# Performance work log

Measured on AMD Instinct MI355X. Metric: run time of the kernel, lower is better.

## Reference

```python
import jax, jax.numpy as jnp
import numpy as np

L, H, C, DH, FF = 6, 8, 512, 64, 2048
B, T, S = 64, 128, 128
EPS = 1e-5


def setup_inputs() -> dict:
    key = jax.random.key(0)
    ks = jax.random.split(key, 20)
    sc = 0.02
    def w(k, shape):
        return jax.random.normal(k, shape, dtype=jnp.float32) * sc
    inp = {
        "x": jax.random.normal(ks[0], (B, T, C), dtype=jnp.float32),
        "encoder_output": jax.random.normal(ks[1], (B, S, C), dtype=jnp.float32),
        # per-head self-attention projections, stacked over layers and heads
        "sa_wq": w(ks[2], (L, H, C, DH)), "sa_bq": w(ks[3], (L, H, DH)),
        "sa_wk": w(ks[4], (L, H, C, DH)), "sa_bk": w(ks[5], (L, H, DH)),
        "sa_wv": w(ks[6], (L, H, C, DH)), "sa_bv": w(ks[7], (L, H, DH)),
        # per-head cross-attention projections
        "ca_wq": w(ks[8], (L, H, C, DH)), "ca_bq": w(ks[9], (L, H, DH)),
        "ca_wk": w(ks[10], (L, H, C, DH)), "ca_bk": w(ks[11], (L, H, DH)),
        "ca_wv": w(ks[12], (L, H, C, DH)), "ca_bv": w(ks[13], (L, H, DH)),
        # feed-forward
        "ff_w1": w(ks[14], (L, C, FF)), "ff_b1": w(ks[15], (L, FF)),
        "ff_w2": w(ks[16], (L, FF, C)), "ff_b2": w(ks[17], (L, C)),
    }
    return inp


def _layer_norm_2d(x):
    # F.layer_norm(x, (T, C)): normalize jointly over last two dims, no affine
    mu = jnp.mean(x, axis=(1, 2), keepdims=True)
    var = jnp.var(x, axis=(1, 2), keepdims=True)
    return (x - mu) * jax.lax.rsqrt(var + EPS)


def _mha(qx, kvx, wq, bq, wk, bk, wv, bv):
    # wq/wk/wv: [H, C, DH]; per-head projections, vectorized over heads.
    q = jnp.einsum("btc,hcd->bhtd", qx, wq) + bq[:, None, :]
    k = jnp.einsum("bsc,hcd->bhsd", kvx, wk) + bk[:, None, :]
    v = jnp.einsum("bsc,hcd->bhsd", kvx, wv) + bv[:, None, :]
    scores = jax.nn.softmax(jnp.einsum("bhtd,bhsd->bhts", q, k) * (DH ** -0.5), axis=-1)
    out = jnp.einsum("bhts,bhsd->bhtd", scores, v)
    b, h, t, d = out.shape  # concat heads along feature dim
    return out.transpose(0, 2, 1, 3).reshape(b, t, h * d)


def reference(x, encoder_output, sa_wq, sa_bq, sa_wk, sa_bk, sa_wv, sa_bv,
              ca_wq, ca_bq, ca_wk, ca_bk, ca_wv, ca_bv,
              ff_w1, ff_b1, ff_w2, ff_b2):
    for l in range(L):
        # masked MHA (note: original code never applies the causal mask)
        x = x + _mha(x, x, sa_wq[l], sa_bq[l], sa_wk[l], sa_bk[l], sa_wv[l], sa_bv[l])
        x = _layer_norm_2d(x)
        # cross attention: q from decoder, k/v from encoder output
        x = x + _mha(x, encoder_output, ca_wq[l], ca_bq[l], ca_wk[l], ca_bk[l], ca_wv[l], ca_bv[l])
        x = _layer_norm_2d(x)
        # feed-forward
        h = jax.nn.relu(jnp.einsum("btc,cf->btf", x, ff_w1[l]) + ff_b1[l])
        x = x + (jnp.einsum("btf,fc->btc", h, ff_w2[l]) + ff_b2[l])
        x = _layer_norm_2d(x)
    return x
```

## Files before the change

kernel.cpp:

```cpp
#include <hip/hip_runtime.h>
#include <hip/hip_bf16.h>


typedef __bf16 bf16;
typedef bf16 bf16x8 __attribute__((ext_vector_type(8)));
typedef float f32x4 __attribute__((ext_vector_type(4)));

#define MFMA16(a, b, c) __builtin_amdgcn_mfma_f32_16x16x32_bf16(a, b, c, 0, 0, 0)

#define GLL16(gsrc, ldst)                                                          \
    __builtin_amdgcn_global_load_lds(                                              \
        (const __attribute__((address_space(1))) void*)(gsrc),                     \
        (__attribute__((address_space(3))) void*)(ldst), 16, 0, 0)

static constexpr int L_ = 6, C_ = 512, FF_ = 2048;
static constexpr int B_ = 64, T_ = 128;
static constexpr int M_ = B_ * T_;
static constexpr float LNINV = 1.f / 65536.f;
static constexpr float EPS_ = 1e-5f;

__global__ __launch_bounds__(256) void zero_part(float* __restrict__ p) {
    for (int i = threadIdx.x; i < 18 * 64 * 2; i += 256) p[i] = 0.f;
}

__global__ __launch_bounds__(256) void init_x(
    const float* __restrict__ xin, float* __restrict__ y, bf16* __restrict__ yb)
{
    const size_t i = ((size_t)blockIdx.x * 256 + threadIdx.x) * 8;
    float4 f0 = *(const float4*)(xin + i);
    float4 f1 = *(const float4*)(xin + i + 4);
    *(float4*)(y + i) = f0;
    *(float4*)(y + i + 4) = f1;
    bf16x8 v = {(bf16)f0.x, (bf16)f0.y, (bf16)f0.z, (bf16)f0.w,
                (bf16)f1.x, (bf16)f1.y, (bf16)f1.z, (bf16)f1.w};
    *(bf16x8*)(yb + i) = v;
}

__global__ __launch_bounds__(256) void to_bf16(
    const float* __restrict__ in, bf16* __restrict__ out)
{
    const size_t i = ((size_t)blockIdx.x * 256 + threadIdx.x) * 8;
    float4 f0 = *(const float4*)(in + i);
    float4 f1 = *(const float4*)(in + i + 4);
    bf16x8 v = {(bf16)f0.x, (bf16)f0.y, (bf16)f0.z, (bf16)f0.w,
                (bf16)f1.x, (bf16)f1.y, (bf16)f1.z, (bf16)f1.w};
    *(bf16x8*)(out + i) = v;
}

__global__ __launch_bounds__(256) void transpose_f32_bf16(
    const float* __restrict__ src, bf16* __restrict__ dst, int R, int C)
{
    __shared__ alignas(16) float t[64][68];
    const int r0 = blockIdx.y * 64, c0 = blockIdx.x * 64;
    const int tr = threadIdx.x >> 4;
    const int tc = (threadIdx.x & 15) * 4;
#pragma unroll
    for (int ro = 0; ro < 64; ro += 16)
        *(float4*)&t[tr + ro][tc] = *(const float4*)(src + (size_t)(r0 + tr + ro) * C + c0 + tc);
    __syncthreads();
    const int wc = (threadIdx.x & 7) * 8;
#pragma unroll
    for (int po = 0; po < 2; ++po) {
        const int oc = (threadIdx.x >> 3) + po * 32;
        bf16x8 v;
#pragma unroll
        for (int j = 0; j < 8; ++j) v[j] = (bf16)t[wc + j][oc];
        *(bf16x8*)(dst + (size_t)(c0 + oc) * R + r0 + wc) = v;
    }
}

__global__ __launch_bounds__(256) void head_repack(
    const float* __restrict__ sa_wq, const float* __restrict__ sa_wk,
    const float* __restrict__ sa_wv, const float* __restrict__ ca_wq,
    const float* __restrict__ ca_wk, const float* __restrict__ ca_wv,
    bf16* __restrict__ Wsa, bf16* __restrict__ Wcaq, bf16* __restrict__ Wcakv)
{
    __shared__ alignas(16) float t[64][68];
    const int z = blockIdx.z;
    const int type = z / 48, rem = z % 48, l = rem >> 3, h = rem & 7;
    const float* srcs[6] = {sa_wq, sa_wk, sa_wv, ca_wq, ca_wk, ca_wv};
    const float* s = srcs[type] + (size_t)(l * 8 + h) * 512 * 64;
    bf16* d;
    if (type < 3)       d = Wsa   + ((size_t)l * 1536 + type * 512 + h * 64) * 512;
    else if (type == 3) d = Wcaq  + ((size_t)l * 512 + h * 64) * 512;
    else                d = Wcakv + ((size_t)l * 1024 + (type - 4) * 512 + h * 64) * 512;
    const int r0 = blockIdx.y * 64;
    const int tr = threadIdx.x >> 4;
    const int tc = (threadIdx.x & 15) * 4;
#pragma unroll
    for (int ro = 0; ro < 64; ro += 16)
        *(float4*)&t[tr + ro][tc] = *(const float4*)(s + (size_t)(r0 + tr + ro) * 64 + tc);
    __syncthreads();
    const int wc = (threadIdx.x & 7) * 8;
#pragma unroll
    for (int po = 0; po < 2; ++po) {
        const int oc = (threadIdx.x >> 3) + po * 32;
        bf16x8 v;
#pragma unroll
        for (int j = 0; j < 8; ++j) v[j] = (bf16)t[wc + j][oc];
        *(bf16x8*)(d + (size_t)oc * 512 + r0 + wc) = v;
    }
}

__global__ __launch_bounds__(256) void colsum_all(
    const float* __restrict__ sa_wq, const float* __restrict__ sa_wk,
    const float* __restrict__ sa_wv, const float* __restrict__ ca_wq,
    const float* __restrict__ ff_w1,
    float* __restrict__ csA, float* __restrict__ csQ, float* __restrict__ csF)
{
    const int t = blockIdx.x * 256 + threadIdx.x;
    const int l = t >> 12, u = t & 4095;
    float sum = 0.f;
    if (u < 1536) {
        const int p = u >> 9, h = (u >> 6) & 7, d = u & 63;
        const float* w = (p == 0) ? sa_wq : (p == 1) ? sa_wk : sa_wv;
        const float* base = w + (size_t)(l * 8 + h) * 512 * 64 + d;
        for (int c = 0; c < 512; ++c) sum += base[(size_t)c * 64];
        csA[l * 1536 + u] = sum;
    } else if (u < 2048) {
        const int v = u - 1536, h = v >> 6, d = v & 63;
        const float* base = ca_wq + (size_t)(l * 8 + h) * 512 * 64 + d;
        for (int c = 0; c < 512; ++c) sum += base[(size_t)c * 64];
        csQ[l * 512 + v] = sum;
    } else {
        const int f = u - 2048;
        const float* base = ff_w1 + (size_t)l * 512 * 2048 + f;
        for (int c = 0; c < 512; ++c) sum += base[(size_t)c * 2048];
        csF[l * 2048 + f] = sum;
    }
}

template <int MODE, int BM>
__global__ __launch_bounds__(256) void gemm_bt(
    const bf16* __restrict__ A, const bf16* __restrict__ BT,
    const float* __restrict__ b0, const float* __restrict__ b1,
    const float* __restrict__ b2, const float* __restrict__ cs,
    float2* __restrict__ part, int slotPrev, int slotNew,
    bf16* __restrict__ o0, bf16* __restrict__ o1, bf16* __restrict__ o2,
    float* __restrict__ y, bf16* __restrict__ ybf, int N, int K)
{
    constexpr int MI = 4;
    constexpr int NI = (BM == 128) ? 4 : 2;
    __shared__ alignas(16) bf16 as[BM][32];
    __shared__ alignas(16) bf16 bs[128][32];
    const int tid = threadIdx.x, wave = tid >> 6, lane = tid & 63;
    const int m0 = blockIdx.y * BM, n0 = blockIdx.x * 128;
    const int wr = (BM == 128) ? (wave >> 1) * 64 : 0;
    const int wc = (BM == 128) ? (wave & 1) * 64 : wave * 32;
    const int fr = lane & 15, fq = lane >> 4;
    const int srow = lane >> 2, schunk = (lane & 3) * 8;

    float mu = 0.f, rstd = 1.f;
    if (slotPrev >= 0) {
        float2 p = part[slotPrev * 64 + (m0 >> 7)];
        mu = p.x * LNINV;
        rstd = rsqrtf(p.y * LNINV - mu * mu + EPS_);
    }

    const bf16* pa = A + (size_t)(m0 + wave * 16 + srow) * K + schunk;
    const bf16* pb = BT + (size_t)(n0 + wave * 16 + srow) * K + schunk;
    bf16* lA = &as[wave * 16][0];
    bf16* lB = &bs[wave * 16][0];

    f32x4 acc[MI][NI] = {};
    for (int k0 = 0; k0 < K; k0 += 32) {
        __syncthreads();
        GLL16(pa + k0, lA);
        if constexpr (BM == 128) GLL16(pa + k0 + (size_t)64 * K, lA + 64 * 32);
        GLL16(pb + k0, lB);
        GLL16(pb + k0 + (size_t)64 * K, lB + 64 * 32);
        __syncthreads();
        bf16x8 af[MI], bfv[NI];
#pragma unroll
        for (int mi = 0; mi < MI; ++mi) af[mi] = *(const bf16x8*)&as[wr + mi * 16 + fr][fq * 8];
#pragma unroll
        for (int ni = 0; ni < NI; ++ni) bfv[ni] = *(const bf16x8*)&bs[wc + ni * 16 + fr][fq * 8];
#pragma unroll
        for (int mi = 0; mi < MI; ++mi)
#pragma unroll
            for (int ni = 0; ni < NI; ++ni)
                acc[mi][ni] = MFMA16(af[mi], bfv[ni], acc[mi][ni]);
    }

    float s = 0.f, ss = 0.f;
    const float murs = mu * rstd;
#pragma unroll
    for (int mi = 0; mi < MI; ++mi) {
#pragma unroll
        for (int ni = 0; ni < NI; ++ni) {
            const int n = n0 + wc + ni * 16 + fr;
#pragma unroll
            for (int reg = 0; reg < 4; ++reg) {
                const int r = m0 + wr + mi * 16 + fq * 4 + reg;
                float val = acc[mi][ni][reg];
                if constexpr (MODE == 0) {
                    const int p = n >> 9, hd = n & 511, d = n & 63, hh = (n >> 6) & 7;
                    const int bb = r >> 7, tt = r & 127;
                    const float* bias = (p == 0) ? b0 : (p == 1 ? b1 : b2);
                    val = val * rstd + bias[hd] - murs * cs[n];
                    const size_t bh = (size_t)(bb * 8 + hh);
                    if (p == 0)      o0[(bh * 128 + tt) * 64 + d] = (bf16)val;
                    else if (p == 1) o1[(bh * 128 + tt) * 64 + d] = (bf16)val;
                    else             o2[(bh * 64 + d) * 128 + tt] = (bf16)val;
                } else if constexpr (MODE == 1) {
                    const int d = n & 63, hh = (n >> 6) & 7;
                    const int bb = r >> 7, tt = r & 127;
                    val = val * rstd + b0[n] - murs * cs[n];
                    o0[((size_t)(bb * 8 + hh) * 128 + tt) * 64 + d] = (bf16)val;
                } else if constexpr (MODE == 2) {
                    const int p = n >> 9, hd = n & 511, d = n & 63, hh = (n >> 6) & 7;
                    const int bb = r >> 7, tt = r & 127;
                    val += (p == 0) ? b1[hd] : b2[hd];
                    const size_t bh = (size_t)(bb * 8 + hh);
                    if (p == 0) o1[(bh * 128 + tt) * 64 + d] = (bf16)val;
                    else        o2[(bh * 64 + d) * 128 + tt] = (bf16)val;
                } else if constexpr (MODE == 3) {
                    val = val * rstd + b0[n] - murs * cs[n];
                    val = fmaxf(val, 0.f);
                    o0[(size_t)r * 2048 + n] = (bf16)val;
                } else {
                    const size_t idx = (size_t)r * 512 + n;
                    const float v = (y[idx] - mu) * rstd + val + b0[n];
                    y[idx] = v;
                    ybf[idx] = (bf16)v;
                    s += v;
                    ss += v * v;
                }
            }
        }
    }
    if constexpr (MODE == 4) {
        for (int off = 32; off; off >>= 1) { s += __shfl_xor(s, off); ss += __shfl_xor(ss, off); }
        __shared__ float rs[4], rss[4];
        if (lane == 0) { rs[wave] = s; rss[wave] = ss; }
        __syncthreads();
        if (tid == 0) {
            float2* dst = &part[slotNew * 64 + (m0 >> 7)];
            atomicAdd(&dst->x, rs[0] + rs[1] + rs[2] + rs[3]);
            atomicAdd(&dst->y, rss[0] + rss[1] + rss[2] + rss[3]);
        }
    }
}

__global__ __launch_bounds__(256) void attn_kernel(
    const bf16* __restrict__ q, const bf16* __restrict__ k,
    const bf16* __restrict__ vT, float* __restrict__ y, bf16* __restrict__ ybf,
    float2* __restrict__ part, int slotPrev, int slotNew)
{
    __shared__ alignas(16) bf16 sP[128][136];
    __shared__ float sInv[128];
    const int bh = blockIdx.x;
    const int bb = bh >> 3, hh = bh & 7;
    const bf16* Q = q + (size_t)bh * 128 * 64;
    const bf16* Kp = k + (size_t)bh * 128 * 64;
    const bf16* V = vT + (size_t)bh * 64 * 128;
    const int tid = threadIdx.x, wave = tid >> 6, lane = tid & 63;
    const int wr = (wave >> 1) * 64, wc = (wave & 1) * 64;
    const int fr = lane & 15, fq = lane >> 4;

    float mu = 0.f, rstd = 1.f;
    if (slotPrev >= 0) {
        float2 p = part[slotPrev * 64 + bb];
        mu = p.x * LNINV;
        rstd = rsqrtf(p.y * LNINV - mu * mu + EPS_);
    }

    f32x4 acc[4][4] = {};
#pragma unroll
    for (int k0 = 0; k0 < 64; k0 += 32) {
        bf16x8 af[4], bfv[4];
#pragma unroll
        for (int mi = 0; mi < 4; ++mi)
            af[mi] = *(const bf16x8*)(Q + (size_t)(wr + mi * 16 + fr) * 64 + k0 + fq * 8);
#pragma unroll
        for (int ni = 0; ni < 4; ++ni)
            bfv[ni] = *(const bf16x8*)(Kp + (size_t)(wc + ni * 16 + fr) * 64 + k0 + fq * 8);
#pragma unroll
        for (int mi = 0; mi < 4; ++mi)
#pragma unroll
            for (int ni = 0; ni < 4; ++ni)
                acc[mi][ni] = MFMA16(af[mi], bfv[ni], acc[mi][ni]);
    }
#pragma unroll
    for (int mi = 0; mi < 4; ++mi)
#pragma unroll
        for (int ni = 0; ni < 4; ++ni)
#pragma unroll
            for (int reg = 0; reg < 4; ++reg)
                sP[wr + mi * 16 + fq * 4 + reg][wc + ni * 16 + fr] =
                    (bf16)(acc[mi][ni][reg] * 0.125f);
    __syncthreads();

    {
        const int r = tid >> 1, h0 = (tid & 1) * 64;
        float mx = -3.0e38f;
        for (int j = 0; j < 64; ++j) mx = fmaxf(mx, (float)sP[r][h0 + j]);
        mx = fmaxf(mx, __shfl_xor(mx, 1));
        float sum = 0.f;
        for (int j = 0; j < 64; ++j) {
            float p = __expf((float)sP[r][h0 + j] - mx);
            sum += p;
            sP[r][h0 + j] = (bf16)p;
        }
        sum += __shfl_xor(sum, 1);
        if ((tid & 1) == 0) sInv[r] = 1.f / sum;
    }
    __syncthreads();

    f32x4 acc2[2][4] = {};
#pragma unroll
    for (int k0 = 0; k0 < 128; k0 += 32) {
        bf16x8 af[2], bfv[4];
#pragma unroll
        for (int mi = 0; mi < 2; ++mi)
            af[mi] = *(const bf16x8*)&sP[wave * 32 + mi * 16 + fr][k0 + fq * 8];
#pragma unroll
        for (int ni = 0; ni < 4; ++ni)
            bfv[ni] = *(const bf16x8*)(V + (size_t)(ni * 16 + fr) * 128 + k0 + fq * 8);
#pragma unroll
        for (int mi = 0; mi < 2; ++mi)
#pragma unroll
            for (int ni = 0; ni < 4; ++ni)
                acc2[mi][ni] = MFMA16(af[mi], bfv[ni], acc2[mi][ni]);
    }

    float s = 0.f, ss = 0.f;
#pragma unroll
    for (int mi = 0; mi < 2; ++mi)
#pragma unroll
        for (int ni = 0; ni < 4; ++ni)
#pragma unroll
            for (int reg = 0; reg < 4; ++reg) {
                const int r = wave * 32 + mi * 16 + fq * 4 + reg;
                const int d = ni * 16 + fr;
                const size_t idx = ((size_t)(bb * 128 + r)) * 512 + hh * 64 + d;
                const float v = (y[idx] - mu) * rstd + acc2[mi][ni][reg] * sInv[r];
                y[idx] = v;
                ybf[idx] = (bf16)v;
                s += v;
                ss += v * v;
            }
    for (int off = 32; off; off >>= 1) { s += __shfl_xor(s, off); ss += __shfl_xor(ss, off); }
    __shared__ float rs[4], rss[4];
    if (lane == 0) { rs[wave] = s; rss[wave] = ss; }
    __syncthreads();
    if (tid == 0) {
        float2* dst = &part[slotNew * 64 + bb];
        atomicAdd(&dst->x, rs[0] + rs[1] + rs[2] + rs[3]);
        atomicAdd(&dst->y, rss[0] + rss[1] + rss[2] + rss[3]);
    }
}

__global__ __launch_bounds__(256) void final_norm(
    const float* __restrict__ y, const float2* __restrict__ part, int slot,
    float* __restrict__ out)
{
    const size_t i = ((size_t)blockIdx.x * 256 + threadIdx.x) * 4;
    const int b = (int)(i >> 16);
    float2 p = part[slot * 64 + b];
    const float mu = p.x * LNINV;
    const float rstd = rsqrtf(p.y * LNINV - mu * mu + EPS_);
    float4 v = *(const float4*)(y + i);
    float4 o = {(v.x - mu) * rstd, (v.y - mu) * rstd, (v.z - mu) * rstd, (v.w - mu) * rstd};
    *(float4*)(out + i) = o;
}

extern "C" void kernel_launch(void* const* d_in, const int* in_sizes, int n_in,
                              void* d_out, int out_size, void* d_ws, size_t ws_size,
                              hipStream_t stream)
{
    (void)in_sizes; (void)n_in; (void)out_size; (void)ws_size;
    const float* x_in  = (const float*)d_in[0];
    const float* enc   = (const float*)d_in[1];
    const float* sa_wq = (const float*)d_in[2];
    const float* sa_bq = (const float*)d_in[3];
    const float* sa_wk = (const float*)d_in[4];
    const float* sa_bk = (const float*)d_in[5];
    const float* sa_wv = (const float*)d_in[6];
    const float* sa_bv = (const float*)d_in[7];
    const float* ca_wq = (const float*)d_in[8];
    const float* ca_bq = (const float*)d_in[9];
    const float* ca_wk = (const float*)d_in[10];
    const float* ca_bk = (const float*)d_in[11];
    const float* ca_wv = (const float*)d_in[12];
    const float* ca_bv = (const float*)d_in[13];
    const float* ff_w1 = (const float*)d_in[14];
    const float* ff_b1 = (const float*)d_in[15];
    const float* ff_w2 = (const float*)d_in[16];
    const float* ff_b2 = (const float*)d_in[17];

    char* wsp = (char*)d_ws;
    auto alloc = [&](size_t bytes) -> char* {
        char* p = wsp;
        wsp += (bytes + 255) & ~(size_t)255;
        return p;
    };
    float* y     = (float*)alloc((size_t)M_ * 512 * 4);
    bf16*  ybf   = (bf16*)alloc((size_t)M_ * 512 * 2);
    bf16*  encbf = (bf16*)alloc((size_t)M_ * 512 * 2);
    char*  shreg = alloc((size_t)M_ * 2048 * 2);
    bf16*  WsaA  = (bf16*)alloc((size_t)L_ * 1536 * 512 * 2);
    bf16*  WcaqA = (bf16*)alloc((size_t)L_ * 512 * 512 * 2);
    bf16*  WcakvA= (bf16*)alloc((size_t)L_ * 1024 * 512 * 2);
    bf16*  Wff1  = (bf16*)alloc((size_t)2048 * 512 * 2);
    bf16*  Wff2  = (bf16*)alloc((size_t)512 * 2048 * 2);
    float* csA   = (float*)alloc((size_t)L_ * 1536 * 4);
    float* csQ   = (float*)alloc((size_t)L_ * 512 * 4);
    float* csF   = (float*)alloc((size_t)L_ * 2048 * 4);
    float2* part = (float2*)alloc(18 * 64 * sizeof(float2));

    bf16* qb   = (bf16*)shreg;
    bf16* kb   = (bf16*)(shreg + (size_t)512 * 128 * 64 * 2);
    bf16* vTb  = (bf16*)(shreg + (size_t)2 * 512 * 128 * 64 * 2);
    bf16* hbuf = (bf16*)shreg;

    dim3 tb(256);
    zero_part<<<1, tb, 0, stream>>>((float*)part);
    init_x<<<2048, tb, 0, stream>>>(x_in, y, ybf);
    to_bf16<<<2048, tb, 0, stream>>>(enc, encbf);
    head_repack<<<dim3(1, 8, 288), tb, 0, stream>>>(sa_wq, sa_wk, sa_wv, ca_wq, ca_wk, ca_wv,
                                                    WsaA, WcaqA, WcakvA);
    colsum_all<<<96, tb, 0, stream>>>(sa_wq, sa_wk, sa_wv, ca_wq, ff_w1, csA, csQ, csF);

    for (int l = 0; l < L_; ++l) {
        transpose_f32_bf16<<<dim3(32, 8, 1), tb, 0, stream>>>(ff_w1 + (size_t)l * 512 * 2048, Wff1, 512, 2048);
        transpose_f32_bf16<<<dim3(8, 32, 1), tb, 0, stream>>>(ff_w2 + (size_t)l * 2048 * 512, Wff2, 2048, 512);
        const int sPrev = (l == 0) ? -1 : (l - 1) * 3 + 2;
        gemm_bt<0, 128><<<dim3(12, 64), tb, 0, stream>>>(ybf, WsaA + (size_t)l * 1536 * 512,
            sa_bq + l * 512, sa_bk + l * 512, sa_bv + l * 512, csA + l * 1536,
            part, sPrev, -1, qb, kb, vTb, nullptr, nullptr, 1536, 512);
        attn_kernel<<<512, tb, 0, stream>>>(qb, kb, vTb, y, ybf, part, sPrev, l * 3 + 0);
        gemm_bt<1, 64><<<dim3(4, 128), tb, 0, stream>>>(ybf, WcaqA + (size_t)l * 512 * 512,
            ca_bq + l * 512, nullptr, nullptr, csQ + l * 512,
            part, l * 3 + 0, -1, qb, nullptr, nullptr, nullptr, nullptr, 512, 512);
        gemm_bt<2, 128><<<dim3(8, 64), tb, 0, stream>>>(encbf, WcakvA + (size_t)l * 1024 * 512,
            nullptr, ca_bk + l * 512, ca_bv + l * 512, nullptr,
            part, -1, -1, nullptr, kb, vTb, nullptr, nullptr, 1024, 512);
        attn_kernel<<<512, tb, 0, stream>>>(qb, kb, vTb, y, ybf, part, l * 3 + 0, l * 3 + 1);
        gemm_bt<3, 128><<<dim3(16, 64), tb, 0, stream>>>(ybf, Wff1,
            ff_b1 + l * 2048, nullptr, nullptr, csF + l * 2048,
            part, l * 3 + 1, -1, hbuf, nullptr, nullptr, nullptr, nullptr, 2048, 512);
        gemm_bt<4, 64><<<dim3(4, 128), tb, 0, stream>>>(hbuf, Wff2,
            ff_b2 + l * 512, nullptr, nullptr, nullptr,
            part, l * 3 + 1, l * 3 + 2, nullptr, nullptr, nullptr, y, ybf, 512, 2048);
    }
    final_norm<<<4096, tb, 0, stream>>>(y, part, 17, (float*)d_out);
}
```

Before: 1.522 ms.

## Double-buffer GEMM K-tiles with swizzled LDS and XCD-aware workgroup remap

The bf16 GEMM mainloop now stages 64-wide K tiles into two LDS buffers. It overlaps the global-to-LDS loads of tile t+2 with MFMA compute on tile t, using a partial vmcnt wait plus barrier instead of two full syncs per 32-wide step. LDS columns are XOR-swizzled by row to cut bank conflicts on the fragment reads. Workgroup IDs are remapped so consecutive tiles land on the same XCD, which should improve L2 reuse. The cost is twice the LDS use per block, which may lower occupancy, and the loop now assumes K is a multiple of 64 and at least 128.

```diff
diff --git a/kernel.cpp b/kernel.cpp
--- a/kernel.cpp
+++ b/kernel.cpp
@@ -141,14 +141,26 @@
 {
     constexpr int MI = 4;
     constexpr int NI = (BM == 128) ? 4 : 2;
-    __shared__ alignas(16) bf16 as[BM][32];
-    __shared__ alignas(16) bf16 bs[128][32];
+    constexpr int AG = BM / 32;
+    constexpr int VG = AG + 4;
+    __shared__ alignas(16) bf16 as[2][BM][64];
+    __shared__ alignas(16) bf16 bs[2][128][64];
     const int tid = threadIdx.x, wave = tid >> 6, lane = tid & 63;
-    const int m0 = blockIdx.y * BM, n0 = blockIdx.x * 128;
+
+    const int gx = gridDim.x;
+    int wgid = blockIdx.y * gx + blockIdx.x;
+    {
+        const int nwg = gx * gridDim.y;
+        const int q = nwg >> 3, r = nwg & 7;
+        const int xcd = wgid & 7, idx = wgid >> 3;
+        wgid = (xcd < r ? xcd * (q + 1) : r * (q + 1) + (xcd - r) * q) + idx;
+    }
+    const int m0 = (wgid / gx) * BM, n0 = (wgid % gx) * 128;
+
     const int wr = (BM == 128) ? (wave >> 1) * 64 : 0;
     const int wc = (BM == 128) ? (wave & 1) * 64 : wave * 32;
     const int fr = lane & 15, fq = lane >> 4;
-    const int srow = lane >> 2, schunk = (lane & 3) * 8;
+    const int xr = fr & 7;
 
     float mu = 0.f, rstd = 1.f;
     if (slotPrev >= 0) {
@@ -157,30 +169,53 @@
         rstd = rsqrtf(p.y * LNINV - mu * mu + EPS_);
     }
 
-    const bf16* pa = A + (size_t)(m0 + wave * 16 + srow) * K + schunk;
-    const bf16* pb = BT + (size_t)(n0 + wave * 16 + srow) * K + schunk;
-    bf16* lA = &as[wave * 16][0];
-    bf16* lB = &bs[wave * 16][0];
+    const int rlane = lane >> 3;
+    const int scol = ((lane & 7) ^ rlane) * 8;
+    const bf16* pa = A + (size_t)(m0 + wave * (BM / 4) + rlane) * K + scol;
+    const bf16* pb = BT + (size_t)(n0 + wave * 32 + rlane) * K + scol;
+
+    auto stage = [&](int buf, int k0) {
+#pragma unroll
+        for (int i = 0; i < AG; ++i)
+            GLL16(pa + k0 + (size_t)(8 * i) * K, &as[buf][wave * (BM / 4) + 8 * i][0]);
+#pragma unroll
+        for (int i = 0; i < 4; ++i)
+            GLL16(pb + k0 + (size_t)(8 * i) * K, &bs[buf][wave * 32 + 8 * i][0]);
+    };
 
     f32x4 acc[MI][NI] = {};
-    for (int k0 = 0; k0 < K; k0 += 32) {
-        __syncthreads();
-        GLL16(pa + k0, lA);
-        if constexpr (BM == 128) GLL16(pa + k0 + (size_t)64 * K, lA + 64 * 32);
-        GLL16(pb + k0, lB);
-        GLL16(pb + k0 + (size_t)64 * K, lB + 64 * 32);
-        __syncthreads();
-        bf16x8 af[MI], bfv[NI];
-#pragma unroll
-        for (int mi = 0; mi < MI; ++mi) af[mi] = *(const bf16x8*)&as[wr + mi * 16 + fr][fq * 8];
-#pragma unroll
-        for (int ni = 0; ni < NI; ++ni) bfv[ni] = *(const bf16x8*)&bs[wc + ni * 16 + fr][fq * 8];
-#pragma unroll
-        for (int mi = 0; mi < MI; ++mi)
+    auto compute = [&](int buf) {
+#pragma unroll
+        for (int kk = 0; kk < 2; ++kk) {
+            bf16x8 af[MI], bfv[NI];
+#pragma unroll
+            for (int mi = 0; mi < MI; ++mi)
+                af[mi] = *(const bf16x8*)&as[buf][wr + mi * 16 + fr][(((kk << 2) + fq) ^ xr) << 3];
 #pragma unroll
             for (int ni = 0; ni < NI; ++ni)
-                acc[mi][ni] = MFMA16(af[mi], bfv[ni], acc[mi][ni]);
-    }
+                bfv[ni] = *(const bf16x8*)&bs[buf][wc + ni * 16 + fr][(((kk << 2) + fq) ^ xr) << 3];
+#pragma unroll
+            for (int mi = 0; mi < MI; ++mi)
+#pragma unroll
+                for (int ni = 0; ni < NI; ++ni)
+                    acc[mi][ni] = MFMA16(af[mi], bfv[ni], acc[mi][ni]);
+        }
+    };
+
+    const int nt = K >> 6;
+    stage(0, 0);
+    stage(1, 64);
+
+    int cur = 0;
+    for (int t = 0; t < nt - 1; ++t) {
+        asm volatile("s_waitcnt vmcnt(%0)\n\ts_barrier" :: "n"(VG) : "memory");
+        compute(cur);
+        __builtin_amdgcn_s_barrier();
+        if (t + 2 < nt) stage(cur, (t + 2) << 6);
+        cur ^= 1;
+    }
+    asm volatile("s_waitcnt vmcnt(0)\n\ts_barrier" ::: "memory");
+    compute(cur);
 
     float s = 0.f, ss = 0.f;
     const float murs = mu * rstd;
```

After: 1.367 ms. -10.2%, faster.
